# Kernel optimization log

Measured on AMD Instinct MI355X. Metric: run time of the kernel, lower is better.

## Reference

```python
import jax, jax.numpy as jnp
import numpy as np
import math

NUM_HEADS = 8
HEAD_DIM = 16  # hidden_features 128 / 8 heads
SCALE = 1.0 / math.sqrt(HEAD_DIM)


def setup_inputs() -> dict:
    key = jax.random.key(0)
    ks = jax.random.split(key, 9)
    N, E, F = 50000, 640000, 128
    node_h = jax.random.normal(ks[0], (N, F), jnp.float32)
    edge_h = jax.random.normal(ks[1], (E, F), jnp.float32)
    # distances kept strictly positive so distance**lambda (and its grad) is well-defined
    distance = jax.random.uniform(ks[2], (E, 1), jnp.float32, minval=0.1, maxval=1.0)
    src = jax.random.randint(ks[3], (E,), 0, N, jnp.int32)
    dst = jax.random.randint(ks[4], (E,), 0, N, jnp.int32)

    def lin(k):
        kw, kb = jax.random.split(k)
        W = jax.random.normal(kw, (F, F), jnp.float32) / math.sqrt(F)
        b = jax.random.normal(kb, (F,), jnp.float32) * 0.02
        return W, b

    Wq, bq = lin(ks[5])
    Wk, bk = lin(ks[6])
    Wv, bv = lin(ks[7])
    Wo, bo = lin(ks[8])
    lam = jnp.array(1.0, jnp.float32)  # attenuation_lambda (clamp in original is a no-op)
    return dict(node_h=node_h, edge_h=edge_h, distance=distance,
                Wq=Wq, bq=bq, Wk=Wk, bk=bk, Wv=Wv, bv=bv, Wo=Wo, bo=bo,
                lam=lam, src=src, dst=dst)


def _segment_softmax(logits, seg, num):
    # softmax over edges sharing the same destination node (DGL mailbox dim=1)
    m = jax.ops.segment_max(logits, seg, num_segments=num)
    m = jax.lax.stop_gradient(jnp.where(jnp.isfinite(m), m, 0.0))
    e = jnp.exp(logits - m[seg])
    den = jax.ops.segment_sum(e, seg, num_segments=num)
    den = jnp.where(den == 0, 1.0, den)  # guard zero in-degree nodes
    return e / den[seg]


def reference(node_h, edge_h, distance, Wq, bq, Wk, bk, Wv, bv, Wo, bo, lam, src, dst):
    N = node_h.shape[0]
    q = (node_h @ Wq.T + bq).reshape(N, NUM_HEADS, HEAD_DIM)
    k = (edge_h @ Wk.T + bk).reshape(-1, NUM_HEADS, HEAD_DIM)
    v = (node_h @ Wv.T + bv).reshape(N, NUM_HEADS, HEAD_DIM)
    qs, qd = q[src], q[dst]                      # [E, H, d] gathers
    in_m = jnp.sum(qs * k, axis=-1)              # [E, H]
    out_m = jnp.sum(qd * k, axis=-1)             # [E, H]
    diag_m = jnp.sum(qs * qd, axis=-1)           # [E, H]
    att = jnp.power(distance, lam)               # [E, 1] power-law attenuation
    score = (_segment_softmax(in_m * SCALE, dst, N)
             + _segment_softmax(out_m * SCALE, dst, N)
             + _segment_softmax(diag_m * SCALE, dst, N)) * att  # [E, H]
    # message value is edges.dst['v'] (as in the original), scatter-sum to dst
    h = jax.ops.segment_sum(score[..., None] * v[dst], dst, num_segments=N)
    h = h.reshape(N, NUM_HEADS * HEAD_DIM)
    out = h @ Wo.T + bo
    return jax.nn.leaky_relu(out, negative_slope=0.1)  # dropout is identity in eval
```

## Files before the change

### kernel.cpp

```cpp
#include <hip/hip_runtime.h>
#include <math.h>

#define H 8
#define FD 128
#define SCALE 0.25f

typedef __attribute__((ext_vector_type(8))) short bf16x8;
typedef __attribute__((ext_vector_type(4))) float f32x4;

__device__ __forceinline__ unsigned short bf_rne(float f) {
    unsigned u = __float_as_uint(f);
    u += 0x7FFFu + ((u >> 16) & 1u);
    return (unsigned short)(u >> 16);
}
__device__ __forceinline__ float bf_to_f(unsigned short s) {
    return __uint_as_float(((unsigned)s) << 16);
}
__device__ __forceinline__ bf16x8 cvt8(const float* __restrict__ p) {
    float4 a = *(const float4*)p;
    float4 b = *(const float4*)(p + 4);
    bf16x8 r;
    r[0] = bf_rne(a.x); r[1] = bf_rne(a.y); r[2] = bf_rne(a.z); r[3] = bf_rne(a.w);
    r[4] = bf_rne(b.x); r[5] = bf_rne(b.y); r[6] = bf_rne(b.z); r[7] = bf_rne(b.w);
    return r;
}

__global__ __launch_bounds__(256) void prep_kernel(
    const float* __restrict__ Wq, const float* __restrict__ Wk,
    const float* __restrict__ Wv, const float* __restrict__ Wo,
    unsigned short* __restrict__ oq, unsigned short* __restrict__ ok,
    unsigned short* __restrict__ ov, unsigned short* __restrict__ oo) {
    int i = blockIdx.x * 256 + threadIdx.x;
    const float* src[4] = {Wq, Wk, Wv, Wo};
    unsigned short* dstp[4] = {oq, ok, ov, oo};
#pragma unroll
    for (int m = 0; m < 4; ++m) {
        float4 w = ((const float4*)src[m])[i];
        ushort4 p = make_ushort4(bf_rne(w.x), bf_rne(w.y), bf_rne(w.z), bf_rne(w.w));
        *(ushort4*)(dstp[m] + i * 4) = p;
    }
}

__global__ __launch_bounds__(256) void qv_kernel(
    const float* __restrict__ X, const unsigned short* __restrict__ Wqb,
    const unsigned short* __restrict__ Wvb, const float* __restrict__ bq,
    const float* __restrict__ bv, unsigned short* __restrict__ qb,
    float* __restrict__ v, int Nrows) {
    const int t = threadIdx.x;
    const int lane = t & 63, wid = t >> 6;
    const int lm = lane & 15, lq = lane >> 4;
    const int r0 = blockIdx.x * 128 + wid * 32;

    bf16x8 a[2][4];
#pragma unroll
    for (int mt = 0; mt < 2; ++mt)
#pragma unroll
        for (int s = 0; s < 4; ++s) {
            int r = r0 + mt * 16 + lm;
            if (r >= Nrows) r = Nrows - 1;
            a[mt][s] = cvt8(X + (size_t)r * FD + s * 32 + lq * 8);
        }
#pragma unroll
    for (int g = 0; g < 2; ++g) {
        const unsigned short* Wb = g ? Wvb : Wqb;
        const float* bias = g ? bv : bq;
        f32x4 acc[2][8];
#pragma unroll
        for (int nt = 0; nt < 8; ++nt) {
            float b = bias[nt * 16 + lm];
#pragma unroll
            for (int mt = 0; mt < 2; ++mt) {
                acc[mt][nt][0] = b; acc[mt][nt][1] = b;
                acc[mt][nt][2] = b; acc[mt][nt][3] = b;
            }
        }
#pragma unroll
        for (int s = 0; s < 4; ++s)
#pragma unroll
            for (int nt = 0; nt < 8; ++nt) {
                bf16x8 bf = *(const bf16x8*)(Wb + (nt * 16 + lm) * FD + s * 32 + lq * 8);
#pragma unroll
                for (int mt = 0; mt < 2; ++mt)
                    acc[mt][nt] = __builtin_amdgcn_mfma_f32_16x16x32_bf16(
                        a[mt][s], bf, acc[mt][nt], 0, 0, 0);
            }
#pragma unroll
        for (int mt = 0; mt < 2; ++mt)
#pragma unroll
            for (int nt = 0; nt < 8; ++nt)
#pragma unroll
                for (int r = 0; r < 4; ++r) {
                    int row = r0 + mt * 16 + lq * 4 + r;
                    if (row >= Nrows) continue;
                    int col = nt * 16 + lm;
                    if (g == 0)
                        qb[(size_t)row * FD + col] = bf_rne(acc[mt][nt][r]);
                    else
                        v[(size_t)row * FD + col] = acc[mt][nt][r];
                }
    }
}

__global__ __launch_bounds__(256) void edge_kernel(
    const float* __restrict__ eh, const unsigned short* __restrict__ Wkb,
    const float* __restrict__ bk, const unsigned short* __restrict__ qb,
    const int* __restrict__ src, const int* __restrict__ dst,
    const float* __restrict__ distance, const float* __restrict__ lam,
    float* __restrict__ den1, float* __restrict__ den2,
    float* __restrict__ den3, float* __restrict__ sc1,
    float* __restrict__ sc2, float* __restrict__ sc3, int E) {
    __shared__ unsigned short lK[128 * 128];
    const int t = threadIdx.x;
    const int e0 = blockIdx.x * 128;
    const int lane = t & 63, wid = t >> 6;
    const int lm = lane & 15, lq = lane >> 4;
    const int wm = wid * 32;

    bf16x8 a[2][4];
#pragma unroll
    for (int mt = 0; mt < 2; ++mt)
#pragma unroll
        for (int s = 0; s < 4; ++s) {
            int e = e0 + wm + mt * 16 + lm;
            if (e >= E) e = E - 1;
            a[mt][s] = cvt8(eh + (size_t)e * FD + s * 32 + lq * 8);
        }
    f32x4 acc[2][8];
#pragma unroll
    for (int nt = 0; nt < 8; ++nt) {
        float b = bk[nt * 16 + lm];
#pragma unroll
        for (int mt = 0; mt < 2; ++mt) {
            acc[mt][nt][0] = b; acc[mt][nt][1] = b;
            acc[mt][nt][2] = b; acc[mt][nt][3] = b;
        }
    }
#pragma unroll
    for (int s = 0; s < 4; ++s)
#pragma unroll
        for (int nt = 0; nt < 8; ++nt) {
            bf16x8 bf = *(const bf16x8*)(Wkb + (nt * 16 + lm) * FD + s * 32 + lq * 8);
#pragma unroll
            for (int mt = 0; mt < 2; ++mt)
                acc[mt][nt] = __builtin_amdgcn_mfma_f32_16x16x32_bf16(
                    a[mt][s], bf, acc[mt][nt], 0, 0, 0);
        }
#pragma unroll
    for (int mt = 0; mt < 2; ++mt)
#pragma unroll
        for (int nt = 0; nt < 8; ++nt)
#pragma unroll
            for (int r = 0; r < 4; ++r) {
                int m = wm + mt * 16 + lq * 4 + r;
                int n = nt * 16 + lm;
                int swb = (n >> 3) ^ (m & 7);
                lK[m * 128 + swb * 8 + (n & 7)] = bf_rne(acc[mt][nt][r]);
            }
    __syncthreads();

    const float lamv = lam[0];
#pragma unroll
    for (int i = 0; i < 4; ++i) {
        int p = i * 256 + t;
        int el = p >> 3, h = p & 7;
        int e = e0 + el;
        if (e >= E) continue;
        int si = src[e], di = dst[e];
        const unsigned short* qsp = qb + (size_t)si * FD + h * 16;
        const unsigned short* qdp = qb + (size_t)di * FD + h * 16;
        bf16x8 qs0 = *(const bf16x8*)qsp;
        bf16x8 qs1 = *(const bf16x8*)(qsp + 8);
        bf16x8 qd0 = *(const bf16x8*)qdp;
        bf16x8 qd1 = *(const bf16x8*)(qdp + 8);
        int swb0 = (2 * h) ^ (el & 7), swb1 = (2 * h + 1) ^ (el & 7);
        bf16x8 k0 = *(const bf16x8*)(lK + el * 128 + swb0 * 8);
        bf16x8 k1 = *(const bf16x8*)(lK + el * 128 + swb1 * 8);
        float pin = 0.f, pot = 0.f, pdg = 0.f;
#pragma unroll
        for (int j = 0; j < 8; ++j) {
            float qsf = bf_to_f((unsigned short)qs0[j]);
            float qdf = bf_to_f((unsigned short)qd0[j]);
            float kf = bf_to_f((unsigned short)k0[j]);
            pin += qsf * kf; pot += qdf * kf; pdg += qsf * qdf;
        }
#pragma unroll
        for (int j = 0; j < 8; ++j) {
            float qsf = bf_to_f((unsigned short)qs1[j]);
            float qdf = bf_to_f((unsigned short)qd1[j]);
            float kf = bf_to_f((unsigned short)k1[j]);
            pin += qsf * kf; pot += qdf * kf; pdg += qsf * qdf;
        }
        float att = __expf(lamv * __logf(distance[e]));
        float e1 = __expf(pin * SCALE);
        float e2 = __expf(pot * SCALE);
        float e3 = __expf(pdg * SCALE);
        int nb = di * H + h;
        atomicAdd(den1 + nb, e1); atomicAdd(sc1 + nb, e1 * att);
        atomicAdd(den2 + nb, e2); atomicAdd(sc2 + nb, e2 * att);
        atomicAdd(den3 + nb, e3); atomicAdd(sc3 + nb, e3 * att);
    }
}

__global__ __launch_bounds__(256) void combine_kernel(
    const float* __restrict__ den1, const float* __restrict__ den2,
    const float* __restrict__ den3, const float* __restrict__ sc1,
    const float* __restrict__ sc2, const float* __restrict__ sc3,
    float* __restrict__ ssum, int NH) {
    int i = blockIdx.x * 256 + threadIdx.x;
    if (i >= NH) return;
    float r = 0.f;
    float d1 = den1[i]; if (d1 != 0.f) r += sc1[i] / d1;
    float d2 = den2[i]; if (d2 != 0.f) r += sc2[i] / d2;
    float d3 = den3[i]; if (d3 != 0.f) r += sc3[i] / d3;
    ssum[i] = r;
}

__global__ __launch_bounds__(256) void out_kernel(
    const float* __restrict__ v, const float* __restrict__ ssum,
    const unsigned short* __restrict__ Wob, const float* __restrict__ bo,
    float* __restrict__ out, int Nrows) {
    const int t = threadIdx.x;
    const int lane = t & 63, wid = t >> 6;
    const int lm = lane & 15, lq = lane >> 4;
    const int r0 = blockIdx.x * 128 + wid * 32;

    bf16x8 a[2][4];
#pragma unroll
    for (int mt = 0; mt < 2; ++mt)
#pragma unroll
        for (int s = 0; s < 4; ++s) {
            int r = r0 + mt * 16 + lm;
            if (r >= Nrows) r = Nrows - 1;
            int k0 = s * 32 + lq * 8;
            float sc = ssum[r * H + (k0 >> 4)];
            const float* p = v + (size_t)r * FD + k0;
            float4 x = *(const float4*)p;
            float4 y = *(const float4*)(p + 4);
            bf16x8 f;
            f[0] = bf_rne(x.x * sc); f[1] = bf_rne(x.y * sc);
            f[2] = bf_rne(x.z * sc); f[3] = bf_rne(x.w * sc);
            f[4] = bf_rne(y.x * sc); f[5] = bf_rne(y.y * sc);
            f[6] = bf_rne(y.z * sc); f[7] = bf_rne(y.w * sc);
            a[mt][s] = f;
        }
    f32x4 acc[2][8];
#pragma unroll
    for (int nt = 0; nt < 8; ++nt) {
        float b = bo[nt * 16 + lm];
#pragma unroll
        for (int mt = 0; mt < 2; ++mt) {
            acc[mt][nt][0] = b; acc[mt][nt][1] = b;
            acc[mt][nt][2] = b; acc[mt][nt][3] = b;
        }
    }
#pragma unroll
    for (int s = 0; s < 4; ++s)
#pragma unroll
        for (int nt = 0; nt < 8; ++nt) {
            bf16x8 bf = *(const bf16x8*)(Wob + (nt * 16 + lm) * FD + s * 32 + lq * 8);
#pragma unroll
            for (int mt = 0; mt < 2; ++mt)
                acc[mt][nt] = __builtin_amdgcn_mfma_f32_16x16x32_bf16(
                    a[mt][s], bf, acc[mt][nt], 0, 0, 0);
        }
#pragma unroll
    for (int mt = 0; mt < 2; ++mt)
#pragma unroll
        for (int nt = 0; nt < 8; ++nt)
#pragma unroll
            for (int r = 0; r < 4; ++r) {
                int row = r0 + mt * 16 + lq * 4 + r;
                if (row >= Nrows) continue;
                int col = nt * 16 + lm;
                float x = acc[mt][nt][r];
                out[(size_t)row * FD + col] = x > 0.f ? x : 0.1f * x;
            }
}

extern "C" void kernel_launch(void* const* d_in, const int* in_sizes, int n_in,
                              void* d_out, int out_size, void* d_ws,
                              size_t ws_size, hipStream_t stream) {
    (void)n_in; (void)out_size; (void)ws_size;
    const float* node_h   = (const float*)d_in[0];
    const float* edge_h   = (const float*)d_in[1];
    const float* distance = (const float*)d_in[2];
    const float* Wq = (const float*)d_in[3];
    const float* bq = (const float*)d_in[4];
    const float* Wk = (const float*)d_in[5];
    const float* bk = (const float*)d_in[6];
    const float* Wv = (const float*)d_in[7];
    const float* bv = (const float*)d_in[8];
    const float* Wo = (const float*)d_in[9];
    const float* bo = (const float*)d_in[10];
    const float* lam = (const float*)d_in[11];
    const int* src = (const int*)d_in[12];
    const int* dst = (const int*)d_in[13];

    int N = in_sizes[0] / FD;
    int E = in_sizes[1] / FD;
    int NH = N * H;

    char* ws = (char*)d_ws;
    unsigned short* Wqb = (unsigned short*)ws; ws += FD * FD * 2;
    unsigned short* Wkb = (unsigned short*)ws; ws += FD * FD * 2;
    unsigned short* Wvb = (unsigned short*)ws; ws += FD * FD * 2;
    unsigned short* Wob = (unsigned short*)ws; ws += FD * FD * 2;
    unsigned short* qb  = (unsigned short*)ws; ws += (size_t)N * FD * 2;
    float* v    = (float*)ws; ws += (size_t)N * FD * 4;
    char* zero_base = ws;
    float* den1 = (float*)ws; ws += (size_t)NH * 4;
    float* den2 = (float*)ws; ws += (size_t)NH * 4;
    float* den3 = (float*)ws; ws += (size_t)NH * 4;
    float* sc1  = (float*)ws; ws += (size_t)NH * 4;
    float* sc2  = (float*)ws; ws += (size_t)NH * 4;
    float* sc3  = (float*)ws; ws += (size_t)NH * 4;
    float* ssum = (float*)ws; ws += (size_t)NH * 4;

    hipMemsetAsync(zero_base, 0, (size_t)6 * NH * 4, stream);

    prep_kernel<<<16, 256, 0, stream>>>(Wq, Wk, Wv, Wo, Wqb, Wkb, Wvb, Wob);

    int nb = (N + 127) / 128;
    qv_kernel<<<nb, 256, 0, stream>>>(node_h, Wqb, Wvb, bq, bv, qb, v, N);

    int ebl = (E + 127) / 128;
    edge_kernel<<<ebl, 256, 0, stream>>>(edge_h, Wkb, bk, qb, src, dst,
                                         distance, lam,
                                         den1, den2, den3, sc1, sc2, sc3, E);

    combine_kernel<<<(NH + 255) / 256, 256, 0, stream>>>(
        den1, den2, den3, sc1, sc2, sc3, ssum, NH);

    out_kernel<<<nb, 256, 0, stream>>>(v, ssum, Wob, bo, (float*)d_out, N);
}
```

Measured before the change: 674.0 us.

## Split edge kernel into chunked K-projection GEMM and per-head attention kernels

Replaces the fused edge kernel, which did the K projection and the attention scoring in one pass, with two kernels run over chunks of edges. The first writes the bf16 K projection into workspace and the second computes the scores and accumulates them atomically, using one thread per edge-head. It also changes the accumulator layout from node-major to head-major (h*N+di), which is meant to spread out the atomics. The cost is an extra write and read of K through workspace plus more kernel launches; the old fused kernel is kept as a fallback when workspace is too small.

```diff
diff --git a/kernel.cpp b/kernel.cpp
--- a/kernel.cpp
+++ b/kernel.cpp
@@ -101,6 +101,101 @@
     }
 }
 
+__global__ __launch_bounds__(256) void kproj_kernel(
+    const float* __restrict__ X, const unsigned short* __restrict__ Wkb,
+    const float* __restrict__ bk, unsigned short* __restrict__ kb, int Nrows) {
+    const int t = threadIdx.x;
+    const int lane = t & 63, wid = t >> 6;
+    const int lm = lane & 15, lq = lane >> 4;
+    const int r0 = blockIdx.x * 128 + wid * 32;
+
+    bf16x8 a[2][4];
+#pragma unroll
+    for (int mt = 0; mt < 2; ++mt)
+#pragma unroll
+        for (int s = 0; s < 4; ++s) {
+            int r = r0 + mt * 16 + lm;
+            if (r >= Nrows) r = Nrows - 1;
+            a[mt][s] = cvt8(X + (size_t)r * FD + s * 32 + lq * 8);
+        }
+    f32x4 acc[2][8];
+#pragma unroll
+    for (int nt = 0; nt < 8; ++nt) {
+        float b = bk[nt * 16 + lm];
+#pragma unroll
+        for (int mt = 0; mt < 2; ++mt) {
+            acc[mt][nt][0] = b; acc[mt][nt][1] = b;
+            acc[mt][nt][2] = b; acc[mt][nt][3] = b;
+        }
+    }
+#pragma unroll
+    for (int s = 0; s < 4; ++s)
+#pragma unroll
+        for (int nt = 0; nt < 8; ++nt) {
+            bf16x8 bf = *(const bf16x8*)(Wkb + (nt * 16 + lm) * FD + s * 32 + lq * 8);
+#pragma unroll
+            for (int mt = 0; mt < 2; ++mt)
+                acc[mt][nt] = __builtin_amdgcn_mfma_f32_16x16x32_bf16(
+                    a[mt][s], bf, acc[mt][nt], 0, 0, 0);
+        }
+#pragma unroll
+    for (int mt = 0; mt < 2; ++mt)
+#pragma unroll
+        for (int nt = 0; nt < 8; ++nt)
+#pragma unroll
+            for (int r = 0; r < 4; ++r) {
+                int row = r0 + mt * 16 + lq * 4 + r;
+                if (row >= Nrows) continue;
+                int col = nt * 16 + lm;
+                kb[(size_t)row * FD + col] = bf_rne(acc[mt][nt][r]);
+            }
+}
+
+__global__ __launch_bounds__(256) void attn_kernel(
+    const unsigned short* __restrict__ kb, const unsigned short* __restrict__ qb,
+    const int* __restrict__ src, const int* __restrict__ dst,
+    const float* __restrict__ distance, const float* __restrict__ lam,
+    float* __restrict__ den1, float* __restrict__ den2,
+    float* __restrict__ den3, float* __restrict__ sc1,
+    float* __restrict__ sc2, float* __restrict__ sc3, int Ec, int N) {
+    int p = blockIdx.x * 256 + threadIdx.x;
+    if (p >= Ec * H) return;
+    int el = p >> 3, h = p & 7;
+    int si = src[el], di = dst[el];
+    const unsigned short* kp  = kb + (size_t)el * FD + h * 16;
+    const unsigned short* qsp = qb + (size_t)si * FD + h * 16;
+    const unsigned short* qdp = qb + (size_t)di * FD + h * 16;
+    bf16x8 k0  = *(const bf16x8*)kp;
+    bf16x8 k1  = *(const bf16x8*)(kp + 8);
+    bf16x8 qs0 = *(const bf16x8*)qsp;
+    bf16x8 qs1 = *(const bf16x8*)(qsp + 8);
+    bf16x8 qd0 = *(const bf16x8*)qdp;
+    bf16x8 qd1 = *(const bf16x8*)(qdp + 8);
+    float pin = 0.f, pot = 0.f, pdg = 0.f;
+#pragma unroll
+    for (int j = 0; j < 8; ++j) {
+        float qsf = bf_to_f((unsigned short)qs0[j]);
+        float qdf = bf_to_f((unsigned short)qd0[j]);
+        float kf  = bf_to_f((unsigned short)k0[j]);
+        pin += qsf * kf; pot += qdf * kf; pdg += qsf * qdf;
+    }
+#pragma unroll
+    for (int j = 0; j < 8; ++j) {
+        float qsf = bf_to_f((unsigned short)qs1[j]);
+        float qdf = bf_to_f((unsigned short)qd1[j]);
+        float kf  = bf_to_f((unsigned short)k1[j]);
+        pin += qsf * kf; pot += qdf * kf; pdg += qsf * qdf;
+    }
+    float att = __expf(lam[0] * __logf(distance[el]));
+    float e1 = __expf(pin * SCALE);
+    float e2 = __expf(pot * SCALE);
+    float e3 = __expf(pdg * SCALE);
+    int nb = h * N + di;
+    atomicAdd(den1 + nb, e1); atomicAdd(sc1 + nb, e1 * att);
+    atomicAdd(den2 + nb, e2); atomicAdd(sc2 + nb, e2 * att);
+    atomicAdd(den3 + nb, e3); atomicAdd(sc3 + nb, e3 * att);
+}
+
 __global__ __launch_bounds__(256) void edge_kernel(
     const float* __restrict__ eh, const unsigned short* __restrict__ Wkb,
     const float* __restrict__ bk, const unsigned short* __restrict__ qb,
@@ -108,7 +203,7 @@
     const float* __restrict__ distance, const float* __restrict__ lam,
     float* __restrict__ den1, float* __restrict__ den2,
     float* __restrict__ den3, float* __restrict__ sc1,
-    float* __restrict__ sc2, float* __restrict__ sc3, int E) {
+    float* __restrict__ sc2, float* __restrict__ sc3, int E, int N) {
     __shared__ unsigned short lK[128 * 128];
     const int t = threadIdx.x;
     const int e0 = blockIdx.x * 128;
@@ -194,7 +289,7 @@
         float e1 = __expf(pin * SCALE);
         float e2 = __expf(pot * SCALE);
         float e3 = __expf(pdg * SCALE);
-        int nb = di * H + h;
+        int nb = h * N + di;
         atomicAdd(den1 + nb, e1); atomicAdd(sc1 + nb, e1 * att);
         atomicAdd(den2 + nb, e2); atomicAdd(sc2 + nb, e2 * att);
         atomicAdd(den3 + nb, e3); atomicAdd(sc3 + nb, e3 * att);
@@ -232,7 +327,7 @@
             int r = r0 + mt * 16 + lm;
             if (r >= Nrows) r = Nrows - 1;
             int k0 = s * 32 + lq * 8;
-            float sc = ssum[r * H + (k0 >> 4)];
+            float sc = ssum[(k0 >> 4) * Nrows + r];
             const float* p = v + (size_t)r * FD + k0;
             float4 x = *(const float4*)p;
             float4 y = *(const float4*)(p + 4);
@@ -280,7 +375,7 @@
 extern "C" void kernel_launch(void* const* d_in, const int* in_sizes, int n_in,
                               void* d_out, int out_size, void* d_ws,
                               size_t ws_size, hipStream_t stream) {
-    (void)n_in; (void)out_size; (void)ws_size;
+    (void)n_in; (void)out_size;
     const float* node_h   = (const float*)d_in[0];
     const float* edge_h   = (const float*)d_in[1];
     const float* distance = (const float*)d_in[2];
@@ -315,6 +410,7 @@
     float* sc2  = (float*)ws; ws += (size_t)NH * 4;
     float* sc3  = (float*)ws; ws += (size_t)NH * 4;
     float* ssum = (float*)ws; ws += (size_t)NH * 4;
+    unsigned short* kb = (unsigned short*)ws;
 
     hipMemsetAsync(zero_base, 0, (size_t)6 * NH * 4, stream);
 
@@ -323,10 +419,30 @@
     int nb = (N + 127) / 128;
     qv_kernel<<<nb, 256, 0, stream>>>(node_h, Wqb, Wvb, bq, bv, qb, v, N);
 
-    int ebl = (E + 127) / 128;
-    edge_kernel<<<ebl, 256, 0, stream>>>(edge_h, Wkb, bk, qb, src, dst,
-                                         distance, lam,
-                                         den1, den2, den3, sc1, sc2, sc3, E);
+    size_t used = (size_t)(ws - (char*)d_ws);
+    size_t avail = ws_size > used ? ws_size - used : 0;
+    size_t cap = avail / ((size_t)FD * 2);
+    size_t per = 327680;
+    if (cap < per) per = cap & ~(size_t)127;
+
+    if (per >= 128) {
+        if (per > (size_t)E) per = (size_t)E;
+        for (size_t s0 = 0; s0 < (size_t)E; s0 += per) {
+            int ce = (int)(((size_t)E - s0) < per ? ((size_t)E - s0) : per);
+            int kblocks = (ce + 127) / 128;
+            kproj_kernel<<<kblocks, 256, 0, stream>>>(
+                edge_h + s0 * FD, Wkb, bk, kb, ce);
+            int ablocks = (int)(((long long)ce * H + 255) / 256);
+            attn_kernel<<<ablocks, 256, 0, stream>>>(
+                kb, qb, src + s0, dst + s0, distance + s0, lam,
+                den1, den2, den3, sc1, sc2, sc3, ce, N);
+        }
+    } else {
+        int ebl = (E + 127) / 128;
+        edge_kernel<<<ebl, 256, 0, stream>>>(
+            edge_h, Wkb, bk, qb, src, dst, distance, lam,
+            den1, den2, den3, sc1, sc2, sc3, E, N);
+    }
 
     combine_kernel<<<(NH + 255) / 256, 256, 0, stream>>>(
         den1, den2, den3, sc1, sc2, sc3, ssum, NH);
```

Measured after the change: 2.053 ms. 3.05x slower.
